# Optimization experiments

Measured on AMD Instinct MI355X. Metric: run time of the kernel, lower is better.

## Reference

```python
import jax, jax.numpy as jnp
import numpy as np

N, D, H, L = 16384, 512, 64, 7  # nodes, feature dim, hidden, num labels


def setup_inputs() -> dict:
    key = jax.random.key(0)
    ks = jax.random.split(key, 6)
    matrix = jax.random.randint(ks[0], (N, N), 0, 2).astype(jnp.float32)  # dense binary adjacency
    x_features = jax.random.normal(ks[1], (N, D), dtype=jnp.float32)
    x_labels = jax.random.randint(ks[2], (N, L), 0, 2).astype(jnp.int32)  # multi-hot labels
    W2 = jax.random.normal(ks[3], (D, H), dtype=jnp.float32) / np.float32(np.sqrt(D))
    b2 = jnp.zeros((H,), jnp.float32)
    Wp = jax.random.normal(ks[4], (D, L), dtype=jnp.float32) / np.float32(np.sqrt(D))
    bp = jnp.zeros((L,), jnp.float32)
    return {"matrix": matrix, "x_features": x_features, "W2": W2, "b2": b2,
            "Wp": Wp, "bp": bp, "x_labels": x_labels, "index": 123, "flag": 2}


def reference(matrix, x_features, W2, b2, Wp, bp, x_labels, index, flag):
    # Implements the flag != 1 path (trans2 -> labelwise aggregation -> maxpool -> predict).
    assert flag == 2
    z = x_features @ W2 + b2                      # [N, 64]  (trans2 over all nodes)
    row = matrix[index]                           # [N] binary neighbor mask of node `index`
    deg = matrix.sum(axis=1)                      # [N] degrees of all nodes
    # para_j = 1/sqrt(deg_j * deg_index) for neighbors, 0 otherwise (row is the mask)
    para = row / jnp.sqrt(deg * row.sum())        # [N]
    lab = x_labels.astype(z.dtype)                # [N, 7]
    # label-wise degree-normalized neighbor aggregation: tmp_a[i] = sum_j para_j * lab[j,i] * z[j]
    tmp_a = jnp.einsum('n,nl,nd->ld', para, lab, z)   # [7, 64]
    h = jax.nn.relu(jnp.concatenate([z[index], tmp_a.reshape(-1)])[None, :])  # [1, 512]
    # stack + MaxPool1d(2) over the pair == elementwise max
    h_combi = jnp.maximum(x_features[index][None, :], h)  # [1, 512]
    out = h_combi @ Wp + bp                        # [1, 7]
    return out
```

## Files before the change

### kernel.cpp

```cpp
#include <hip/hip_runtime.h>

#define NN 16384
#define DD 512
#define HH 64
#define LL 7

#define WS_CNT  0
#define WS_C    8
#define WS_G    16
#define WS_NBR  4096
#define WS_QV   20480

__global__ void k_prep(const float* __restrict__ matrix,
                       const int* __restrict__ pidx,
                       const float* __restrict__ bp,
                       int* __restrict__ count,
                       int* __restrict__ nbr,
                       float* __restrict__ g,
                       float* __restrict__ c,
                       float* __restrict__ out) {
    __shared__ int lds_wt[16];
    __shared__ int lds_woff[16];
    int t = threadIdx.x;
    int lane = t & 63;
    int wid = t >> 6;

    for (int i = t; i < LL * DD; i += 1024) g[i] = 0.f;
    if (t < LL) { c[t] = 0.f; out[t] = bp[t]; }

    int idx = *pidx;
    const float4* r4 = (const float4*)(matrix + (size_t)idx * NN);
    float4 v[4];
    #pragma unroll
    for (int q = 0; q < 4; ++q) v[q] = r4[t * 4 + q];

    unsigned m16 = 0;
    int cnt_t = 0;
    #pragma unroll
    for (int q = 0; q < 4; ++q) {
        const float* f = &v[q].x;
        #pragma unroll
        for (int cc = 0; cc < 4; ++cc)
            if (f[cc] != 0.f) { m16 |= 1u << (q * 4 + cc); ++cnt_t; }
    }

    int inc = cnt_t;
    #pragma unroll
    for (int off = 1; off < 64; off <<= 1) {
        int u = __shfl_up(inc, off);
        if (lane >= off) inc += u;
    }
    if (lane == 63) lds_wt[wid] = inc;
    __syncthreads();
    if (t == 0) {
        int run = 0;
        #pragma unroll
        for (int w = 0; w < 16; ++w) { int x = lds_wt[w]; lds_woff[w] = run; run += x; }
        *count = run;
    }
    __syncthreads();

    int offb = lds_woff[wid] + inc - cnt_t;
    int w = 0;
    #pragma unroll
    for (int bit = 0; bit < 16; ++bit) {
        if (m16 & (1u << bit)) nbr[offb + (w++)] = t * 16 + bit;
    }
}

__global__ void k_deg(const float* __restrict__ matrix,
                      const int* __restrict__ count,
                      const int* __restrict__ nbr,
                      float* __restrict__ qv) {
    __shared__ float sdata[4];
    int t = threadIdx.x;
    int lane = t & 63;
    int wid = t >> 6;
    int cnt = *count;
    for (int i = blockIdx.x; i < cnt; i += gridDim.x) {
        int j = nbr[i];
        const float4* r4 = (const float4*)(matrix + (size_t)j * NN);
        float v0 = 0.f, v1 = 0.f, v2 = 0.f, v3 = 0.f;
        #pragma unroll
        for (int it = 0; it < 4; ++it) {
            float4 a  = r4[t + (it * 4 + 0) * 256];
            float4 b  = r4[t + (it * 4 + 1) * 256];
            float4 cc = r4[t + (it * 4 + 2) * 256];
            float4 d  = r4[t + (it * 4 + 3) * 256];
            v0 += a.x + a.y + a.z + a.w;
            v1 += b.x + b.y + b.z + b.w;
            v2 += cc.x + cc.y + cc.z + cc.w;
            v3 += d.x + d.y + d.z + d.w;
        }
        float v = (v0 + v1) + (v2 + v3);
        #pragma unroll
        for (int off = 32; off > 0; off >>= 1)
            v += __shfl_down(v, off);
        if (lane == 0) sdata[wid] = v;
        __syncthreads();
        if (t == 0) {
            float deg = (sdata[0] + sdata[1]) + (sdata[2] + sdata[3]);
            qv[i] = rsqrtf(deg);
        }
        __syncthreads();
    }
}

__global__ void k_agg(const float* __restrict__ xf,
                      const int* __restrict__ lab,
                      const int* __restrict__ count,
                      const int* __restrict__ nbr,
                      const float* __restrict__ qv,
                      float* __restrict__ g,
                      float* __restrict__ c) {
    int t = threadIdx.x;
    int d0 = t * 2;
    int cnt = *count;
    float2 acc[LL];
    #pragma unroll
    for (int l = 0; l < LL; ++l) acc[l] = make_float2(0.f, 0.f);
    float cacc[LL] = {0.f, 0.f, 0.f, 0.f, 0.f, 0.f, 0.f};

    for (int base = 0; base < cnt; base += 1024) {
        int ii[4];
        bool act[4];
        int jj[4];
        float qq[4];
        float2 xv[4];
        #pragma unroll
        for (int k = 0; k < 4; ++k) {
            ii[k] = base + blockIdx.x + k * 256;
            act[k] = ii[k] < cnt;
        }
        #pragma unroll
        for (int k = 0; k < 4; ++k) {
            jj[k] = act[k] ? nbr[ii[k]] : 0;
            qq[k] = act[k] ? qv[ii[k]] : 0.f;
        }
        #pragma unroll
        for (int k = 0; k < 4; ++k)
            xv[k] = act[k] ? *(const float2*)(xf + (size_t)jj[k] * DD + d0)
                           : make_float2(0.f, 0.f);
        #pragma unroll
        for (int k = 0; k < 4; ++k) {
            float wl[LL];
            #pragma unroll
            for (int l = 0; l < LL; ++l)
                wl[l] = qq[k] * (float)lab[jj[k] * LL + l];
            #pragma unroll
            for (int l = 0; l < LL; ++l) {
                acc[l].x = fmaf(wl[l], xv[k].x, acc[l].x);
                acc[l].y = fmaf(wl[l], xv[k].y, acc[l].y);
            }
            if (t == 0) {
                #pragma unroll
                for (int l = 0; l < LL; ++l) cacc[l] += wl[l];
            }
        }
    }
    #pragma unroll
    for (int l = 0; l < LL; ++l) {
        atomicAdd(&g[l * DD + d0],     acc[l].x);
        atomicAdd(&g[l * DD + d0 + 1], acc[l].y);
    }
    if (t == 0) {
        #pragma unroll
        for (int l = 0; l < LL; ++l) atomicAdd(&c[l], cacc[l]);
    }
}

__global__ void k_final(const float* __restrict__ xf,
                        const float* __restrict__ W2,
                        const float* __restrict__ b2,
                        const float* __restrict__ Wp,
                        const int* __restrict__ pidx,
                        const int* __restrict__ count,
                        const float* __restrict__ g,
                        const float* __restrict__ c,
                        float* __restrict__ out) {
    __shared__ float out_acc[LL];
    int t = threadIdx.x;
    int p = blockIdx.x * 64 + (t >> 2);
    int sub = t & 3;
    int idx = *pidx;
    float sc = rsqrtf((float)(*count));

    const float* src;
    float bias;
    int h;
    if (p < HH) {
        src = xf + (size_t)idx * DD;
        h = p;
        bias = b2[p];
    } else {
        int l = (p - HH) >> 6;
        h = (p - HH) & 63;
        src = g + l * DD;
        bias = c[l] * b2[h];
    }
    float s0 = 0.f, s1 = 0.f, s2 = 0.f, s3 = 0.f;
    int dbase = sub * 128;
    #pragma unroll 8
    for (int d = 0; d < 128; d += 4) {
        s0 = fmaf(src[dbase + d],     W2[(dbase + d)     * HH + h], s0);
        s1 = fmaf(src[dbase + d + 1], W2[(dbase + d + 1) * HH + h], s1);
        s2 = fmaf(src[dbase + d + 2], W2[(dbase + d + 2) * HH + h], s2);
        s3 = fmaf(src[dbase + d + 3], W2[(dbase + d + 3) * HH + h], s3);
    }
    float v = (s0 + s1) + (s2 + s3);
    v += __shfl_down(v, 2);
    v += __shfl_down(v, 1);

    if (t < LL) out_acc[t] = 0.f;
    __syncthreads();

    if (sub == 0) {
        float val = v + bias;
        if (p >= HH) val *= sc;
        float relu_v = val > 0.f ? val : 0.f;
        float hc = fmaxf(xf[(size_t)idx * DD + p], relu_v);
        #pragma unroll
        for (int o = 0; o < LL; ++o)
            atomicAdd(&out_acc[o], hc * Wp[p * LL + o]);
    }
    __syncthreads();
    if (t < LL) atomicAdd(&out[t], out_acc[t]);
}

extern "C" void kernel_launch(void* const* d_in, const int* in_sizes, int n_in,
                              void* d_out, int out_size, void* d_ws, size_t ws_size,
                              hipStream_t stream) {
    const float* matrix = (const float*)d_in[0];
    const float* xf     = (const float*)d_in[1];
    const float* W2     = (const float*)d_in[2];
    const float* b2     = (const float*)d_in[3];
    const float* Wp     = (const float*)d_in[4];
    const float* bp     = (const float*)d_in[5];
    const int*   lab    = (const int*)d_in[6];
    const int*   pidx   = (const int*)d_in[7];
    float* outp = (float*)d_out;
    float* wsf  = (float*)d_ws;

    k_prep<<<1, 1024, 0, stream>>>(matrix, pidx, bp,
                                   (int*)(wsf + WS_CNT), (int*)(wsf + WS_NBR),
                                   wsf + WS_G, wsf + WS_C, outp);
    k_deg<<<8192, 256, 0, stream>>>(matrix, (const int*)(wsf + WS_CNT),
                                    (const int*)(wsf + WS_NBR), wsf + WS_QV);
    k_agg<<<256, 256, 0, stream>>>(xf, lab, (const int*)(wsf + WS_CNT),
                                   (const int*)(wsf + WS_NBR), wsf + WS_QV,
                                   wsf + WS_G, wsf + WS_C);
    k_final<<<8, 256, 0, stream>>>(xf, W2, b2, Wp, pidx,
                                   (const int*)(wsf + WS_CNT),
                                   wsf + WS_G, wsf + WS_C, outp);
}
```

Measured before the change: 159.8 us.

## Drop neighbor compaction kernel; mask per-row degree work and use deterministic partials

Removes the single-block prep kernel that compacted the neighbor list. Each degree block now checks its own mask entry and returns early for non-neighbors, and the degree row reads use nontemporal loads. Aggregation walks all nodes strided by block, skips zero weights, and writes per-block partial sums instead of atomics. The final kernel reduces those partials in LDS. The change removes a serial launch and the atomics, at the cost of launching 16384 degree blocks and scanning qv for every node.

```diff
diff --git a/kernel.cpp b/kernel.cpp
--- a/kernel.cpp
+++ b/kernel.cpp
@@ -4,168 +4,127 @@
 #define DD 512
 #define HH 64
 #define LL 7
-
-#define WS_CNT  0
-#define WS_C    8
-#define WS_G    16
-#define WS_NBR  4096
-#define WS_QV   20480
-
-__global__ void k_prep(const float* __restrict__ matrix,
-                       const int* __restrict__ pidx,
-                       const float* __restrict__ bp,
-                       int* __restrict__ count,
-                       int* __restrict__ nbr,
-                       float* __restrict__ g,
-                       float* __restrict__ c,
-                       float* __restrict__ out) {
-    __shared__ int lds_wt[16];
-    __shared__ int lds_woff[16];
+#define NAGG 256
+#define JPB  (NN / NAGG)
+
+typedef float f32x4 __attribute__((ext_vector_type(4)));
+
+#define WS_QV 0
+#define WS_S  16384
+#define WS_CP 16400
+#define WS_GP 20480
+
+__global__ void k_deg(const float* __restrict__ matrix,
+                      const int* __restrict__ pidx,
+                      float* __restrict__ qv) {
+    __shared__ float sdata[4];
+    int j = blockIdx.x;
     int t = threadIdx.x;
     int lane = t & 63;
     int wid = t >> 6;
-
-    for (int i = t; i < LL * DD; i += 1024) g[i] = 0.f;
-    if (t < LL) { c[t] = 0.f; out[t] = bp[t]; }
-
     int idx = *pidx;
-    const float4* r4 = (const float4*)(matrix + (size_t)idx * NN);
-    float4 v[4];
-    #pragma unroll
-    for (int q = 0; q < 4; ++q) v[q] = r4[t * 4 + q];
-
-    unsigned m16 = 0;
-    int cnt_t = 0;
-    #pragma unroll
-    for (int q = 0; q < 4; ++q) {
-        const float* f = &v[q].x;
-        #pragma unroll
-        for (int cc = 0; cc < 4; ++cc)
-            if (f[cc] != 0.f) { m16 |= 1u << (q * 4 + cc); ++cnt_t; }
-    }
-
-    int inc = cnt_t;
-    #pragma unroll
-    for (int off = 1; off < 64; off <<= 1) {
-        int u = __shfl_up(inc, off);
-        if (lane >= off) inc += u;
-    }
-    if (lane == 63) lds_wt[wid] = inc;
+    float m = matrix[(size_t)idx * NN + j];
+    if (m == 0.f) {
+        if (t == 0) qv[j] = 0.f;
+        return;
+    }
+    const f32x4* r4 = (const f32x4*)(matrix + (size_t)j * NN);
+    float v0 = 0.f, v1 = 0.f, v2 = 0.f, v3 = 0.f;
+    #pragma unroll
+    for (int it = 0; it < 4; ++it) {
+        f32x4 a  = __builtin_nontemporal_load(&r4[t + (it * 4 + 0) * 256]);
+        f32x4 b  = __builtin_nontemporal_load(&r4[t + (it * 4 + 1) * 256]);
+        f32x4 cc = __builtin_nontemporal_load(&r4[t + (it * 4 + 2) * 256]);
+        f32x4 d  = __builtin_nontemporal_load(&r4[t + (it * 4 + 3) * 256]);
+        v0 += a.x + a.y + a.z + a.w;
+        v1 += b.x + b.y + b.z + b.w;
+        v2 += cc.x + cc.y + cc.z + cc.w;
+        v3 += d.x + d.y + d.z + d.w;
+    }
+    float v = (v0 + v1) + (v2 + v3);
+    #pragma unroll
+    for (int off = 32; off > 0; off >>= 1)
+        v += __shfl_down(v, off);
+    if (lane == 0) sdata[wid] = v;
     __syncthreads();
     if (t == 0) {
-        int run = 0;
-        #pragma unroll
-        for (int w = 0; w < 16; ++w) { int x = lds_wt[w]; lds_woff[w] = run; run += x; }
-        *count = run;
-    }
-    __syncthreads();
-
-    int offb = lds_woff[wid] + inc - cnt_t;
-    int w = 0;
-    #pragma unroll
-    for (int bit = 0; bit < 16; ++bit) {
-        if (m16 & (1u << bit)) nbr[offb + (w++)] = t * 16 + bit;
-    }
-}
-
-__global__ void k_deg(const float* __restrict__ matrix,
-                      const int* __restrict__ count,
-                      const int* __restrict__ nbr,
-                      float* __restrict__ qv) {
-    __shared__ float sdata[4];
+        float deg = (sdata[0] + sdata[1]) + (sdata[2] + sdata[3]);
+        qv[j] = rsqrtf(deg);
+    }
+}
+
+__global__ void k_agg(const float* __restrict__ matrix,
+                      const float* __restrict__ xf,
+                      const int* __restrict__ lab,
+                      const int* __restrict__ pidx,
+                      const float* __restrict__ bp,
+                      const float* __restrict__ qv,
+                      float* __restrict__ gpart,
+                      float* __restrict__ cpart,
+                      float* __restrict__ Sout,
+                      float* __restrict__ out) {
+    __shared__ float sS[4];
     int t = threadIdx.x;
-    int lane = t & 63;
-    int wid = t >> 6;
-    int cnt = *count;
-    for (int i = blockIdx.x; i < cnt; i += gridDim.x) {
-        int j = nbr[i];
-        const float4* r4 = (const float4*)(matrix + (size_t)j * NN);
-        float v0 = 0.f, v1 = 0.f, v2 = 0.f, v3 = 0.f;
-        #pragma unroll
-        for (int it = 0; it < 4; ++it) {
-            float4 a  = r4[t + (it * 4 + 0) * 256];
-            float4 b  = r4[t + (it * 4 + 1) * 256];
-            float4 cc = r4[t + (it * 4 + 2) * 256];
-            float4 d  = r4[t + (it * 4 + 3) * 256];
-            v0 += a.x + a.y + a.z + a.w;
-            v1 += b.x + b.y + b.z + b.w;
-            v2 += cc.x + cc.y + cc.z + cc.w;
-            v3 += d.x + d.y + d.z + d.w;
-        }
-        float v = (v0 + v1) + (v2 + v3);
-        #pragma unroll
-        for (int off = 32; off > 0; off >>= 1)
-            v += __shfl_down(v, off);
-        if (lane == 0) sdata[wid] = v;
-        __syncthreads();
-        if (t == 0) {
-            float deg = (sdata[0] + sdata[1]) + (sdata[2] + sdata[3]);
-            qv[i] = rsqrtf(deg);
-        }
-        __syncthreads();
-    }
-}
-
-__global__ void k_agg(const float* __restrict__ xf,
-                      const int* __restrict__ lab,
-                      const int* __restrict__ count,
-                      const int* __restrict__ nbr,
-                      const float* __restrict__ qv,
-                      float* __restrict__ g,
-                      float* __restrict__ c) {
-    int t = threadIdx.x;
+    int b = blockIdx.x;
     int d0 = t * 2;
-    int cnt = *count;
     float2 acc[LL];
     #pragma unroll
     for (int l = 0; l < LL; ++l) acc[l] = make_float2(0.f, 0.f);
     float cacc[LL] = {0.f, 0.f, 0.f, 0.f, 0.f, 0.f, 0.f};
 
-    for (int base = 0; base < cnt; base += 1024) {
-        int ii[4];
-        bool act[4];
+    #pragma unroll 1
+    for (int trip = 0; trip < JPB / 4; ++trip) {
         int jj[4];
         float qq[4];
-        float2 xv[4];
         #pragma unroll
         for (int k = 0; k < 4; ++k) {
-            ii[k] = base + blockIdx.x + k * 256;
-            act[k] = ii[k] < cnt;
+            jj[k] = b + (trip * 4 + k) * NAGG;
+            qq[k] = qv[jj[k]];
         }
         #pragma unroll
         for (int k = 0; k < 4; ++k) {
-            jj[k] = act[k] ? nbr[ii[k]] : 0;
-            qq[k] = act[k] ? qv[ii[k]] : 0.f;
-        }
-        #pragma unroll
-        for (int k = 0; k < 4; ++k)
-            xv[k] = act[k] ? *(const float2*)(xf + (size_t)jj[k] * DD + d0)
-                           : make_float2(0.f, 0.f);
-        #pragma unroll
-        for (int k = 0; k < 4; ++k) {
-            float wl[LL];
-            #pragma unroll
-            for (int l = 0; l < LL; ++l)
-                wl[l] = qq[k] * (float)lab[jj[k] * LL + l];
-            #pragma unroll
-            for (int l = 0; l < LL; ++l) {
-                acc[l].x = fmaf(wl[l], xv[k].x, acc[l].x);
-                acc[l].y = fmaf(wl[l], xv[k].y, acc[l].y);
-            }
-            if (t == 0) {
+            if (qq[k] != 0.f) {
+                float2 xv = *(const float2*)(xf + (size_t)jj[k] * DD + d0);
+                float wl[LL];
+                #pragma unroll
+                for (int l = 0; l < LL; ++l)
+                    wl[l] = qq[k] * (float)lab[jj[k] * LL + l];
+                #pragma unroll
+                for (int l = 0; l < LL; ++l) {
+                    acc[l].x = fmaf(wl[l], xv.x, acc[l].x);
+                    acc[l].y = fmaf(wl[l], xv.y, acc[l].y);
+                }
                 #pragma unroll
                 for (int l = 0; l < LL; ++l) cacc[l] += wl[l];
             }
         }
     }
     #pragma unroll
-    for (int l = 0; l < LL; ++l) {
-        atomicAdd(&g[l * DD + d0],     acc[l].x);
-        atomicAdd(&g[l * DD + d0 + 1], acc[l].y);
-    }
+    for (int l = 0; l < LL; ++l)
+        *(float2*)(gpart + ((size_t)b * LL + l) * DD + d0) = acc[l];
     if (t == 0) {
         #pragma unroll
-        for (int l = 0; l < LL; ++l) atomicAdd(&c[l], cacc[l]);
+        for (int l = 0; l < LL; ++l) cpart[b * 8 + l] = cacc[l];
+    }
+    if (b == 0) {
+        int idx = *pidx;
+        const f32x4* r4 = (const f32x4*)(matrix + (size_t)idx * NN);
+        float v = 0.f;
+        #pragma unroll
+        for (int it = 0; it < 16; ++it) {
+            f32x4 a = r4[t + it * 256];
+            v += a.x + a.y + a.z + a.w;
+        }
+        #pragma unroll
+        for (int off = 32; off > 0; off >>= 1)
+            v += __shfl_down(v, off);
+        if ((t & 63) == 0) sS[t >> 6] = v;
+        __syncthreads();
+        if (t == 0) {
+            Sout[0] = (sS[0] + sS[1]) + (sS[2] + sS[3]);
+            #pragma unroll
+            for (int l = 0; l < LL; ++l) out[l] = bp[l];
+        }
     }
 }
 
@@ -174,32 +133,49 @@
                         const float* __restrict__ b2,
                         const float* __restrict__ Wp,
                         const int* __restrict__ pidx,
-                        const int* __restrict__ count,
-                        const float* __restrict__ g,
-                        const float* __restrict__ c,
+                        const float* __restrict__ gpart,
+                        const float* __restrict__ cpart,
+                        const float* __restrict__ Sf,
                         float* __restrict__ out) {
+    __shared__ float gl[DD];
+    __shared__ float csd[4];
+    __shared__ float csum_s;
     __shared__ float out_acc[LL];
     int t = threadIdx.x;
-    int p = blockIdx.x * 64 + (t >> 2);
+    int b = blockIdx.x;
+    int lane = t & 63;
+    int wid = t >> 6;
+    int idx = *pidx;
+
+    if (b >= 1) {
+        int l = b - 1;
+        float2 s = make_float2(0.f, 0.f);
+        const float* gbase = gpart + (size_t)l * DD + t * 2;
+        #pragma unroll 8
+        for (int pb = 0; pb < NAGG; ++pb) {
+            float2 v = *(const float2*)(gbase + (size_t)pb * (LL * DD));
+            s.x += v.x; s.y += v.y;
+        }
+        gl[t * 2] = s.x;
+        gl[t * 2 + 1] = s.y;
+        float cv = cpart[t * 8 + l];
+        #pragma unroll
+        for (int off = 32; off > 0; off >>= 1)
+            cv += __shfl_down(cv, off);
+        if (lane == 0) csd[wid] = cv;
+    }
+    if (t < LL) out_acc[t] = 0.f;
+    __syncthreads();
+    if (b >= 1 && t == 0)
+        csum_s = (csd[0] + csd[1]) + (csd[2] + csd[3]);
+    __syncthreads();
+
+    int p = b * 64 + (t >> 2);
     int sub = t & 3;
-    int idx = *pidx;
-    float sc = rsqrtf((float)(*count));
-
-    const float* src;
-    float bias;
-    int h;
-    if (p < HH) {
-        src = xf + (size_t)idx * DD;
-        h = p;
-        bias = b2[p];
-    } else {
-        int l = (p - HH) >> 6;
-        h = (p - HH) & 63;
-        src = g + l * DD;
-        bias = c[l] * b2[h];
-    }
+    int h = (b == 0) ? p : (p - HH) & 63;
+    int dbase = sub * 128;
+    const float* src = (b == 0) ? (xf + (size_t)idx * DD) : gl;
     float s0 = 0.f, s1 = 0.f, s2 = 0.f, s3 = 0.f;
-    int dbase = sub * 128;
     #pragma unroll 8
     for (int d = 0; d < 128; d += 4) {
         s0 = fmaf(src[dbase + d],     W2[(dbase + d)     * HH + h], s0);
@@ -211,12 +187,14 @@
     v += __shfl_down(v, 2);
     v += __shfl_down(v, 1);
 
-    if (t < LL) out_acc[t] = 0.f;
-    __syncthreads();
-
     if (sub == 0) {
-        float val = v + bias;
-        if (p >= HH) val *= sc;
+        float val;
+        if (b == 0) {
+            val = v + b2[p];
+        } else {
+            float sc = rsqrtf(Sf[0]);
+            val = (v + csum_s * b2[h]) * sc;
+        }
         float relu_v = val > 0.f ? val : 0.f;
         float hc = fmaxf(xf[(size_t)idx * DD + p], relu_v);
         #pragma unroll
@@ -241,15 +219,9 @@
     float* outp = (float*)d_out;
     float* wsf  = (float*)d_ws;
 
-    k_prep<<<1, 1024, 0, stream>>>(matrix, pidx, bp,
-                                   (int*)(wsf + WS_CNT), (int*)(wsf + WS_NBR),
-                                   wsf + WS_G, wsf + WS_C, outp);
-    k_deg<<<8192, 256, 0, stream>>>(matrix, (const int*)(wsf + WS_CNT),
-                                    (const int*)(wsf + WS_NBR), wsf + WS_QV);
-    k_agg<<<256, 256, 0, stream>>>(xf, lab, (const int*)(wsf + WS_CNT),
-                                   (const int*)(wsf + WS_NBR), wsf + WS_QV,
-                                   wsf + WS_G, wsf + WS_C);
+    k_deg<<<NN, 256, 0, stream>>>(matrix, pidx, wsf + WS_QV);
+    k_agg<<<NAGG, 256, 0, stream>>>(matrix, xf, lab, pidx, bp, wsf + WS_QV,
+                                    wsf + WS_GP, wsf + WS_CP, wsf + WS_S, outp);
     k_final<<<8, 256, 0, stream>>>(xf, W2, b2, Wp, pidx,
-                                   (const int*)(wsf + WS_CNT),
-                                   wsf + WS_G, wsf + WS_C, outp);
-}
+                                   wsf + WS_GP, wsf + WS_CP, wsf + WS_S, outp);
+}
```

New measurement: 135.4 us. 1.18x faster.
